# Kernel tuning notes

Measured on AMD Instinct MI355X. Metric: run time of the kernel, lower is better.

The kernel has to match this reference:

```python
import jax, jax.numpy as jnp
import numpy as np

LN_EPS = 1e-5
EPS = 1e-8
MESH_LR = 1.0
MESH_ITERS = 4
SH_ITERS = 5
SA_ITERS = 3


def build_grid(res):
    ranges = [np.linspace(0.0, 1.0, num=r) for r in res]
    g = np.stack(np.meshgrid(*ranges, indexing='ij'), axis=-1)
    g = g.reshape(res[0], res[1], -1)[None]
    return jnp.asarray(np.concatenate([g, 1.0 - g], axis=-1).astype(np.float32))  # [1,H,W,4]


def layer_norm(x, w, b):
    m = jnp.mean(x, axis=-1, keepdims=True)
    v = jnp.var(x, axis=-1, keepdims=True)
    return (x - m) * jax.lax.rsqrt(v + LN_EPS) * w + b


def l2norm(x):
    n = jnp.linalg.norm(x, axis=-1, keepdims=True)
    return x / jnp.maximum(n, 1e-12)  # matches F.normalize eps


def conv_relu(x, w, b, stride):
    y = jax.lax.conv_general_dilated(x, w, (stride, stride), [(2, 2), (2, 2)],
                                     dimension_numbers=('NCHW', 'OIHW', 'NCHW'))
    return jax.nn.relu(y + b[None, :, None, None])


def sinkhorn(C, a, b, u=None, v=None, n_iters=SH_ITERS):
    # log-domain Sinkhorn; C: [B,N,S] cost, a: [B,N], b: [B,S] marginals
    p = -C
    log_a, log_b = jnp.log(a), jnp.log(b)
    if u is None:
        u = jnp.zeros_like(a)
    if v is None:
        v = jnp.zeros_like(b)
    for _ in range(n_iters):
        u = log_a - jax.nn.logsumexp(p + v[:, None, :], axis=2)
        v = log_b - jax.nn.logsumexp(p + u[:, :, None], axis=1)
    pi = jnp.exp(p + u[:, :, None] + v[:, None, :])
    return pi, u, v


def minimize_entropy_of_sinkhorn(C0, a, b, mesh_lr=MESH_LR, n_mesh_iters=MESH_ITERS):
    # gradient descent on the cost matrix to minimize entropy of the transport plan
    def ent(C, u, v):
        pi, u2, v2 = sinkhorn(C, a, b, u=u, v=v)
        e = jnp.mean(-jnp.sum(pi * jnp.log(pi + EPS), axis=(1, 2)))
        return e, (u2, v2)

    grad_fn = jax.grad(ent, has_aux=True)
    u, v = jnp.zeros_like(a), jnp.zeros_like(b)
    C = C0
    for _ in range(n_mesh_iters):
        g, (u, v) = grad_fn(C, u, v)
        C = C - mesh_lr * g
    return C, u, v


def gru_cell(x, h, wih, whh, bih, bhh):
    gi = x @ wih.T + bih
    gh = h @ whh.T + bhh
    ir, iz, inn = jnp.split(gi, 3, axis=-1)
    hr, hz, hn = jnp.split(gh, 3, axis=-1)
    r = jax.nn.sigmoid(ir + hr)
    z = jax.nn.sigmoid(iz + hz)
    n = jnp.tanh(inn + r * hn)
    return (1.0 - z) * n + z * h


def setup_inputs() -> dict:
    key = jax.random.key(0)
    ks = iter(jax.random.split(key, 48))

    def nrm(shape, fan_in):
        return jax.random.normal(next(ks), shape, jnp.float32) / np.sqrt(fan_in).astype(np.float32)

    B, d, S, HID = 16, 64, 8, 128
    z = lambda *s: jnp.zeros(s, jnp.float32)
    o = lambda *s: jnp.ones(s, jnp.float32)
    inp = {
        'image': jax.random.normal(next(ks), (B, 3, 128, 128), jnp.float32),
        'slots_noise': jax.random.normal(next(ks), (B, S, d), jnp.float32),
        'conv1_w': nrm((64, 3, 5, 5), 75), 'conv1_b': z(64),
        'conv2_w': nrm((64, 64, 5, 5), 1600), 'conv2_b': z(64),
        'conv3_w': nrm((64, 64, 5, 5), 1600), 'conv3_b': z(64),
        'conv4_w': nrm((64, 64, 5, 5), 1600), 'conv4_b': z(64),
        'pos_w': nrm((d, 4), 4), 'pos_b': z(d),
        'mlp1_w': nrm((d, d), d), 'mlp1_b': z(d),
        'mlp2_w': nrm((d, d), d), 'mlp2_b': z(d),
        'ln_in_w': o(d), 'ln_in_b': z(d),
        'wk': nrm((d, d), d), 'wv': nrm((d, d), d), 'wq': nrm((d, d), d),
        'mwi_w': nrm((1, d), d), 'mwi_b': z(1),
        'mws_w': nrm((1, d), d), 'mws_b': z(1),
        'ln_sl_w': o(d), 'ln_sl_b': z(d),
        'gru_wih': nrm((3 * d, d), d), 'gru_whh': nrm((3 * d, d), d),
        'gru_bih': z(3 * d), 'gru_bhh': z(3 * d),
        'ln_ff_w': o(d), 'ln_ff_b': z(d),
        'fc1_w': nrm((HID, d), d), 'fc1_b': z(HID),
        'fc2_w': nrm((d, HID), HID), 'fc2_b': z(d),
        'slots_mu': nrm((1, 1, d), d),
        'slots_sigma': jax.random.uniform(next(ks), (1, 1, d), jnp.float32),
        'num_slots': 8,
    }
    return inp


def reference(image, slots_noise, conv1_w, conv1_b, conv2_w, conv2_b, conv3_w, conv3_b,
              conv4_w, conv4_b, pos_w, pos_b, mlp1_w, mlp1_b, mlp2_w, mlp2_b,
              ln_in_w, ln_in_b, wk, wv, wq, mwi_w, mwi_b, mws_w, mws_b,
              ln_sl_w, ln_sl_b, gru_wih, gru_whh, gru_bih, gru_bhh,
              ln_ff_w, ln_ff_b, fc1_w, fc1_b, fc2_w, fc2_b,
              slots_mu, slots_sigma, num_slots):
    B = image.shape[0]
    d = slots_mu.shape[-1]
    # --- CNN encoder (strided_convs=True => latent 32x32) ---
    x = conv_relu(image, conv1_w, conv1_b, 1)
    x = conv_relu(x, conv2_w, conv2_b, 2)
    x = conv_relu(x, conv3_w, conv3_b, 2)
    x = conv_relu(x, conv4_w, conv4_b, 1)          # [B,64,32,32]
    x = x.transpose(0, 2, 3, 1)                    # [B,32,32,64]
    grid = build_grid((32, 32))                    # [1,32,32,4]
    x = x + (grid @ pos_w.T + pos_b)               # soft position embed
    feat = x.reshape(B, -1, d)                     # [B,1024,64]
    # --- pre-slot-attention MLP ---
    feat = jax.nn.relu(feat @ mlp1_w.T + mlp1_b) @ mlp2_w.T + mlp2_b
    # --- slot attention with MESH-Sinkhorn ---
    n_s = num_slots
    slots = slots_mu + (jnp.abs(slots_sigma) + EPS) * slots_noise  # Normal rsample
    inp = layer_norm(feat, ln_in_w, ln_in_b)
    k = inp @ wk.T
    v = inp @ wv.T
    a = jax.nn.softmax((inp @ mwi_w.T + mwi_b).squeeze(-1), axis=-1) * n_s  # [B,N]
    kn = l2norm(k)
    attn = None
    for _ in range(SA_ITERS):
        slots_prev = slots
        s = layer_norm(slots, ln_sl_w, ln_sl_b)
        bm = jax.nn.softmax((s @ mws_w.T + mws_b).squeeze(-1), axis=-1) * n_s  # [B,S]
        q = s @ wq.T
        C = 1.0 - jnp.einsum('bnd,bsd->bns', kn, l2norm(q))  # cosine distance
        C, p, qq = minimize_entropy_of_sinkhorn(C, a, bm)
        pi, _, _ = sinkhorn(C, a, bm, u=p, v=qq)
        attn = pi.transpose(0, 2, 1)                         # [B,S,N]
        updates = jnp.einsum('bsn,bnd->bsd', attn, v)
        slots = gru_cell(updates.reshape(-1, d), slots_prev.reshape(-1, d),
                         gru_wih, gru_whh, gru_bih, gru_bhh).reshape(B, n_s, d)
        h = layer_norm(slots, ln_ff_w, ln_ff_b)
        slots = slots + (jax.nn.relu(h @ fc1_w.T + fc1_b) @ fc2_w.T + fc2_b)
    return slots, attn
```

## Files before the change

### kernel.cpp

```cpp
#include <hip/hip_runtime.h>
#include <hip/hip_bf16.h>


#define LN_EPS 1e-5f
#define SEPS 1e-8f
#define LN8 2.0794415416798357f

__device__ inline float ldf(float x) { return x; }
__device__ inline float ldf(__hip_bfloat16 x) { return __bfloat162float(x); }
__device__ inline void stf(float* p, float v) { *p = v; }
__device__ inline void stf(__hip_bfloat16* p, float v) { *p = __float2bfloat16(v); }

__device__ inline float wmaxall(float v) {
#pragma unroll
  for (int o = 32; o; o >>= 1) v = fmaxf(v, __shfl_down(v, o));
  return __shfl(v, 0);
}
__device__ inline float wsumall(float v) {
#pragma unroll
  for (int o = 32; o; o >>= 1) v += __shfl_down(v, o);
  return __shfl(v, 0);
}
__device__ inline int wsumi(int v) {
#pragma unroll
  for (int o = 32; o; o >>= 1) v += __shfl_down(v, o);
  return __shfl(v, 0);
}
__device__ inline float fast_sigmoid(float x) { return 1.f / (1.f + __expf(-x)); }
__device__ inline float fast_tanh(float x) { return 1.f - 2.f / (__expf(2.f * x) + 1.f); }

__global__ __launch_bounds__(64) void sniff_kernel(const unsigned int* __restrict__ img,
                                                   int* __restrict__ flag) {
  int cnt = 0;
  for (int i = threadIdx.x; i < 512; i += 64) {
    unsigned lo = img[i] & 0xFFFFu;
    int e = (int)((lo >> 7) & 0xFFu);
    cnt += (e >= 96 && e <= 140) ? 1 : 0;
  }
  cnt = wsumi(cnt);
  if (threadIdx.x == 0) *flag = (cnt >= 300) ? 1 : 0;
}

struct CvtArgs {
  const void* src[39];
  long off[40];
};

__global__ __launch_bounds__(256) void convert_kernel(CvtArgs a, const int* __restrict__ flag,
                                                      float* __restrict__ dst, long total) {
  const int isbf = *flag;
  for (long g = (long)blockIdx.x * 256 + threadIdx.x; g < total; g += (long)gridDim.x * 256) {
    int lo = 0, hi = 38;
    while (lo < hi) {
      int mid = (lo + hi + 1) >> 1;
      if (a.off[mid] <= g) lo = mid; else hi = mid - 1;
    }
    long li = g - a.off[lo];
    float v;
    if (isbf) v = __bfloat162float(((const __hip_bfloat16*)a.src[lo])[li]);
    else      v = ((const float*)a.src[lo])[li];
    dst[g] = v;
  }
}

struct TwArgs {
  long soff[9]; long doff[9]; int R[9]; int C[9];
};

__global__ __launch_bounds__(256) void transw_kernel(const float* __restrict__ cvt,
                                                     float* __restrict__ tws, TwArgs a) {
  int m = blockIdx.x;
  const float* S = cvt + a.soff[m];
  float* D = tws + a.doff[m];
  int R = a.R[m], C = a.C[m];
  for (int idx = threadIdx.x; idx < R * C; idx += 256) {
    int i = idx / C, j = idx - i * C;
    D[j * R + i] = S[idx];
  }
}

template <int S, typename TIN, typename TOUT>
__global__ __launch_bounds__(256) void conv5x5(
    const TIN* __restrict__ in, const float* __restrict__ wgt,
    const float* __restrict__ bias, TOUT* __restrict__ out,
    int Cin, int H, int W, int Ho, int Wo, int Cout, int tilesX) {
  constexpr int P = 15 * S + 5;
  constexpr int PP = (S == 1) ? 20 : 40;
  constexpr int NCH = (S == 1) ? 2 : 3;
  constexpr int NP = (P * P + 255) / 256;
  __shared__ __align__(16) float patch[P * PP];
  __shared__ float wt16[25 * 16];
  const int b = blockIdx.z;
  const int ocg = blockIdx.y * 16;
  const int ty0 = (blockIdx.x / tilesX) * 16, tx0 = (blockIdx.x % tilesX) * 16;
  const int og = threadIdx.x >> 6;
  const int r = (threadIdx.x >> 2) & 15;
  const int rx = threadIdx.x & 3;
  const int iy0 = ty0 * S - 2, ix0 = tx0 * S - 2;
  const long HW = (long)H * W;

  int toff[NP], soff[NP];
#pragma unroll
  for (int q = 0; q < NP; q++) {
    int idx = threadIdx.x + 256 * q;
    toff[q] = -1;
    soff[q] = -1;
    if (idx < P * P) {
      int py = idx / P, px = idx - py * P;
      int iy = iy0 + py, ix = ix0 + px;
      int pxs = (S == 2) ? (px ^ (((py >> 1) & 1) << 2)) : px;
      toff[q] = py * PP + pxs;
      if (iy >= 0 && iy < H && ix >= 0 && ix < W) soff[q] = iy * W + ix;
    }
  }
  int wsrc[2];
#pragma unroll
  for (int q = 0; q < 2; q++) {
    int idx = threadIdx.x + 256 * q;
    wsrc[q] = (idx < 400) ? (((ocg + (idx & 15)) * Cin) * 25 + (idx >> 4)) : -1;
  }

  float acc[4][4];
#pragma unroll
  for (int p = 0; p < 4; p++)
#pragma unroll
    for (int j = 0; j < 4; j++) acc[p][j] = 0.f;

  float pr[NP], wr[2];
  {
    const TIN* inp = in + (long)b * Cin * HW;
#pragma unroll
    for (int q = 0; q < NP; q++) pr[q] = (soff[q] >= 0) ? ldf(inp[soff[q]]) : 0.f;
#pragma unroll
    for (int q = 0; q < 2; q++) wr[q] = (wsrc[q] >= 0) ? wgt[wsrc[q]] : 0.f;
  }

  for (int ci = 0; ci < Cin; ++ci) {
    __syncthreads();
#pragma unroll
    for (int q = 0; q < NP; q++)
      if (toff[q] >= 0) patch[toff[q]] = pr[q];
#pragma unroll
    for (int q = 0; q < 2; q++) {
      int idx = threadIdx.x + 256 * q;
      if (idx < 400) wt16[idx] = wr[q];
    }
    __syncthreads();
    if (ci + 1 < Cin) {
      const TIN* inp = in + ((long)b * Cin + ci + 1) * HW;
#pragma unroll
      for (int q = 0; q < NP; q++) pr[q] = (soff[q] >= 0) ? ldf(inp[soff[q]]) : 0.f;
#pragma unroll
      for (int q = 0; q < 2; q++)
        if (wsrc[q] >= 0) wr[q] = wgt[wsrc[q] + (ci + 1) * 25];
    }
#pragma unroll
    for (int ky = 0; ky < 5; ky++) {
      float win[4 * NCH];
      const int row = r * S + ky;
      const float* rb = &patch[row * PP];
      if constexpr (S == 2) {
        const int sw = (row >> 1) & 1;
#pragma unroll
        for (int c = 0; c < NCH; c++) {
          const int g = rx * 2 + c;
          float4 t4 = *(const float4*)(rb + ((g ^ sw) << 2));
          win[4 * c + 0] = t4.x;
          win[4 * c + 1] = t4.y;
          win[4 * c + 2] = t4.z;
          win[4 * c + 3] = t4.w;
        }
      } else {
        const float* bp = rb + rx * 4;
#pragma unroll
        for (int c = 0; c < NCH; c++) {
          float4 t4 = *(const float4*)(bp + 4 * c);
          win[4 * c + 0] = t4.x;
          win[4 * c + 1] = t4.y;
          win[4 * c + 2] = t4.z;
          win[4 * c + 3] = t4.w;
        }
      }
#pragma unroll
      for (int kx = 0; kx < 5; kx++) {
        const float4 wv = *(const float4*)&wt16[(ky * 5 + kx) * 16 + og * 4];
#pragma unroll
        for (int p = 0; p < 4; p++) {
          float iv = win[p * S + kx];
          acc[p][0] += iv * wv.x;
          acc[p][1] += iv * wv.y;
          acc[p][2] += iv * wv.z;
          acc[p][3] += iv * wv.w;
        }
      }
    }
  }
  const int oy = ty0 + r, ox0 = tx0 + rx * 4;
#pragma unroll
  for (int j = 0; j < 4; j++) {
    int oc = ocg + og * 4 + j;
    float bs = bias[oc];
    TOUT* op = &out[(((long)b * Cout + oc) * Ho + oy) * Wo + ox0];
#pragma unroll
    for (int p = 0; p < 4; p++) stf(&op[p], fmaxf(acc[p][j] + bs, 0.f));
  }
}

__global__ __launch_bounds__(64) void token_kernel(
    const float* __restrict__ act4, const float* __restrict__ pos_w,
    const float* __restrict__ pos_b,
    const float* __restrict__ mlp1T, const float* __restrict__ mlp1_b,
    const float* __restrict__ mlp2T, const float* __restrict__ mlp2_b,
    const float* __restrict__ lnin_w, const float* __restrict__ lnin_b,
    const float* __restrict__ wkT, const float* __restrict__ wvT,
    const float* __restrict__ mwi_w, const float* __restrict__ mwi_b,
    float* __restrict__ knT_out, float* __restrict__ v_out, float* __restrict__ lg_out) {
  const int t = blockIdx.x, i = threadIdx.x;
  const int b = t >> 10, nn = t & 1023;
  const int h = nn >> 5, w = nn & 31;
  __shared__ float f[64], h1[64], inp[64];
  {
    float gh = h * (1.f / 31.f), gw = w * (1.f / 31.f);
    float e = gh * pos_w[i * 4 + 0] + gw * pos_w[i * 4 + 1] +
              (1.f - gh) * pos_w[i * 4 + 2] + (1.f - gw) * pos_w[i * 4 + 3] + pos_b[i];
    f[i] = act4[(((long)b * 64 + i) * 32 + h) * 32 + w] + e;
  }
  __syncthreads();
  float acc = 0.f;
  for (int j = 0; j < 64; j++) acc += f[j] * mlp1T[j * 64 + i];
  h1[i] = fmaxf(acc + mlp1_b[i], 0.f);
  __syncthreads();
  acc = 0.f;
  for (int j = 0; j < 64; j++) acc += h1[j] * mlp2T[j * 64 + i];
  float x = acc + mlp2_b[i];
  float m = wsumall(x) * (1.f / 64.f);
  float d0 = x - m;
  float var = wsumall(d0 * d0) * (1.f / 64.f);
  float xin = d0 * rsqrtf(var + LN_EPS) * lnin_w[i] + lnin_b[i];
  inp[i] = xin;
  __syncthreads();
  float kv = 0.f, vv = 0.f;
  for (int j = 0; j < 64; j++) {
    float ij = inp[j];
    kv += ij * wkT[j * 64 + i];
    vv += ij * wvT[j * 64 + i];
  }
  float ss = wsumall(kv * kv);
  knT_out[(long)b * 65536 + i * 1024 + nn] = kv / fmaxf(sqrtf(ss), 1e-12f);
  v_out[(long)t * 64 + i] = vv;
  float lg = wsumall(xin * mwi_w[i]);
  if (i == 0) lg_out[t] = lg + mwi_b[0];
}

__global__ __launch_bounds__(512) void sa_kernel(
    const float* __restrict__ knT_g, const float* __restrict__ v_g,
    const float* __restrict__ la_g, const float* __restrict__ noise,
    const float* __restrict__ mu_w, const float* __restrict__ sg_w,
    const float* __restrict__ lnsl_w, const float* __restrict__ lnsl_b,
    const float* __restrict__ mws_w, const float* __restrict__ mws_b,
    const float* __restrict__ wqT,
    const float* __restrict__ wihT, const float* __restrict__ whhT,
    const float* __restrict__ bih, const float* __restrict__ bhh,
    const float* __restrict__ lnff_w, const float* __restrict__ lnff_b,
    const float* __restrict__ fc1T, const float* __restrict__ fc1_b,
    const float* __restrict__ fc2T, const float* __restrict__ fc2_b,
    float* __restrict__ out) {
  const int b = blockIdx.x, tid = threadIdx.x;
  const int wv = tid >> 6, ln = tid & 63;

  __shared__ float sCt[8192];
  __shared__ float sEc[8192];
  __shared__ float sLa[1024], sELa[1024], sHid[1024];
  __shared__ float sPart[512 * 9];
  __shared__ float sVh[48], sV[8], sEsv[8], sGv[8], sLb[8], sBm[8];
  __shared__ float sC1[8], sEvh[8];
  __shared__ float sSlots[512], sNorm[512], sQn[512], sUpd[512];

  const float* knt = knT_g + (long)b * 65536;
  const float* vf = v_g + (long)b * 65536;
  float sInvH[5][2];
  float gPr[2][8];
  float gInit[2];

  {
    int dd = tid & 63;
    sSlots[tid] = mu_w[dd] + (fabsf(sg_w[dd]) + SEPS) * noise[(long)b * 512 + tid];
  }
  for (int n = tid; n < 1024; n += 512) sLa[n] = la_g[b * 1024 + n];
  __syncthreads();
  {
    float a0 = sLa[tid], a1 = sLa[tid + 512];
    float m0 = wmaxall(fmaxf(a0, a1));
    if (ln == 0) sBm[wv] = m0;
    __syncthreads();
    float M = sBm[0];
#pragma unroll
    for (int s = 1; s < 8; s++) M = fmaxf(M, sBm[s]);
    float e0 = wsumall(__expf(a0 - M) + __expf(a1 - M));
    if (ln == 0) sGv[wv] = e0;
    __syncthreads();
    float SS = 0.f;
#pragma unroll
    for (int s = 0; s < 8; s++) SS += sGv[s];
    float lse = M + __logf(SS);
    float l0 = a0 - lse + LN8, l1 = a1 - lse + LN8;
    sLa[tid] = l0;
    sLa[tid + 512] = l1;
    sELa[tid] = __expf(l0);
    sELa[tid + 512] = __expf(l1);
  }
  __syncthreads();

  for (int it = 0; it < 3; ++it) {
    {
      float x = sSlots[wv * 64 + ln];
      float m = wsumall(x) * (1.f / 64.f);
      float d0 = x - m;
      float var = wsumall(d0 * d0) * (1.f / 64.f);
      float xn = d0 * rsqrtf(var + LN_EPS) * lnsl_w[ln] + lnsl_b[ln];
      sNorm[wv * 64 + ln] = xn;
      float bmv = wsumall(xn * mws_w[ln]);
      if (ln == 0) sBm[wv] = bmv + mws_b[0];
    }
    __syncthreads();
    if (tid == 0) {
      float mx = -1e30f;
      for (int s = 0; s < 8; s++) mx = fmaxf(mx, sBm[s]);
      float ss = 0.f;
      for (int s = 0; s < 8; s++) ss += __expf(sBm[s] - mx);
      float lse = mx + __logf(ss);
      for (int s = 0; s < 8; s++) sLb[s] = sBm[s] - lse + LN8;
    }
    {
      float acc = 0.f;
      for (int j = 0; j < 64; j++) acc += sNorm[wv * 64 + j] * wqT[j * 64 + ln];
      sQn[tid] = acc;
    }
    __syncthreads();
    {
      float qv = sQn[wv * 64 + ln];
      float ss = wsumall(qv * qv);
      sQn[wv * 64 + ln] = qv / fmaxf(sqrtf(ss), 1e-12f);
    }
    if (tid < 8) {
      sV[tid] = 0.f;
      sEsv[tid] = 1.f;
    }
    __syncthreads();

#pragma unroll
    for (int k = 0; k < 2; k++) {
      int n = tid + 512 * k;
      float acc[8];
#pragma unroll
      for (int s = 0; s < 8; s++) acc[s] = 0.f;
      for (int j = 0; j < 64; j++) {
        float kvv = knt[j * 1024 + n];
#pragma unroll
        for (int s = 0; s < 8; s++) acc[s] += kvv * sQn[s * 64 + j];
      }
#pragma unroll
      for (int s = 0; s < 8; s++) {
        float c = 1.f - acc[s];
        sCt[s * 1024 + n] = c;
        sEc[s * 1024 + n] = __expf(-c);
      }
    }
    __syncthreads();

    for (int m = 0; m < 4; m++) {
#pragma unroll
      for (int t = 1; t <= 5; t++) {
        if (t == 1 && tid < 8) sVh[tid] = sV[tid];
        float esv_r[8], part[8];
#pragma unroll
        for (int s = 0; s < 8; s++) { esv_r[s] = sEsv[s]; part[s] = 0.f; }
#pragma unroll
        for (int k = 0; k < 2; k++) {
          int n = tid + 512 * k;
          float ec[8], S = 0.f;
#pragma unroll
          for (int s = 0; s < 8; s++) {
            ec[s] = sEc[s * 1024 + n];
            S += esv_r[s] * ec[s];
          }
          float inv = 1.f / S;
          sInvH[t - 1][k] = inv;
          float w = sELa[n] * inv;
#pragma unroll
          for (int s = 0; s < 8; s++) part[s] += w * ec[s];
        }
#pragma unroll
        for (int s = 0; s < 8; s++) sPart[tid * 9 + s] = part[s];
        __syncthreads();
        {
          int s = wv;
          float acc = 0.f;
#pragma unroll
          for (int q = 0; q < 8; q++) acc += sPart[(ln + 64 * q) * 9 + s];
          acc = wsumall(acc);
          if (ln == 0) {
            float vs = sLb[s] - __logf(acc);
            sV[s] = vs;
            sVh[t * 8 + s] = vs;
            sEsv[s] = __expf(vs);
          }
        }
        __syncthreads();
      }
      {
        float esv_r[8], part[8];
#pragma unroll
        for (int s = 0; s < 8; s++) { esv_r[s] = sEsv[s]; part[s] = 0.f; }
#pragma unroll
        for (int k = 0; k < 2; k++) {
          int n = tid + 512 * k;
          float al = sELa[n] * sInvH[4][k];
          float gul = 0.f;
#pragma unroll
          for (int s = 0; s < 8; s++) {
            float pi = al * esv_r[s] * sEc[s * 1024 + n];
            float gl = -(__logf(pi + SEPS) + pi / (pi + SEPS)) * pi * (1.f / 16.f);
            gPr[k][s] = gl;
            gul += gl;
            part[s] += gl;
          }
          gInit[k] = gul;
        }
#pragma unroll
        for (int s = 0; s < 8; s++) sPart[tid * 9 + s] = part[s];
        __syncthreads();
        {
          int s = wv;
          float acc = 0.f;
#pragma unroll
          for (int q = 0; q < 8; q++) acc += sPart[(ln + 64 * q) * 9 + s];
          acc = wsumall(acc);
          if (ln == 0) {
            sGv[s] = acc;
            sC1[s] = acc * __expf(sVh[40 + s] - sLb[s]);
            sEvh[s] = __expf(sVh[32 + s]);
          }
        }
        __syncthreads();
      }
#pragma unroll
      for (int t = 5; t >= 1; t--) {
        float c1_r[8], evh_r[8], part[8];
#pragma unroll
        for (int s = 0; s < 8; s++) {
          c1_r[s] = sC1[s];
          evh_r[s] = sEvh[s];
          part[s] = 0.f;
        }
#pragma unroll
        for (int k = 0; k < 2; k++) {
          int n = tid + 512 * k;
          float inv = sInvH[t - 1][k];
          float al = sELa[n] * inv;
          float gul = (t == 5) ? gInit[k] : 0.f;
          float ec[8];
#pragma unroll
          for (int s = 0; s < 8; s++) {
            ec[s] = sEc[s * 1024 + n];
            float t2 = al * c1_r[s] * ec[s];
            gPr[k][s] -= t2;
            gul -= t2;
          }
          float bv = gul * inv;
#pragma unroll
          for (int s = 0; s < 8; s++) {
            float pe = bv * ec[s];
            gPr[k][s] -= pe * evh_r[s];
            part[s] += pe;
          }
          if (t == 1) {
#pragma unroll
            for (int s = 0; s < 8; s++) {
              float cn = sCt[s * 1024 + n] + gPr[k][s];
              sCt[s * 1024 + n] = cn;
              sEc[s * 1024 + n] = __expf(-cn);
            }
          }
        }
        if (t > 1) {
#pragma unroll
          for (int s = 0; s < 8; s++) sPart[tid * 9 + s] = part[s];
        }
        if (t == 1 && tid < 8) {
          float vs = sVh[40 + tid];
          sV[tid] = vs;
          sEsv[tid] = __expf(vs);
        }
        __syncthreads();
        if (t > 1) {
          int s = wv;
          float acc = 0.f;
#pragma unroll
          for (int q = 0; q < 8; q++) acc += sPart[(ln + 64 * q) * 9 + s];
          acc = wsumall(acc);
          if (ln == 0) {
            float gn = -evh_r[s] * acc;
            sGv[s] = gn;
            sC1[s] = gn * __expf(sVh[(t - 1) * 8 + s] - sLb[s]);
            sEvh[s] = __expf(sVh[(t - 2) * 8 + s]);
          }
          __syncthreads();
        }
      }
    }

    float invF[2];
    for (int t = 0; t < 5; t++) {
      float esv_r[8], part[8];
#pragma unroll
      for (int s = 0; s < 8; s++) { esv_r[s] = sEsv[s]; part[s] = 0.f; }
#pragma unroll
      for (int k = 0; k < 2; k++) {
        int n = tid + 512 * k;
        float ec[8], S = 0.f;
#pragma unroll
        for (int s = 0; s < 8; s++) {
          ec[s] = sEc[s * 1024 + n];
          S += esv_r[s] * ec[s];
        }
        float inv = 1.f / S;
        invF[k] = inv;
        float w = sELa[n] * inv;
#pragma unroll
        for (int s = 0; s < 8; s++) part[s] += w * ec[s];
      }
#pragma unroll
      for (int s = 0; s < 8; s++) sPart[tid * 9 + s] = part[s];
      __syncthreads();
      {
        int s = wv;
        float acc = 0.f;
#pragma unroll
        for (int q = 0; q < 8; q++) acc += sPart[(ln + 64 * q) * 9 + s];
        acc = wsumall(acc);
        if (ln == 0) {
          float vs = sLb[s] - __logf(acc);
          sV[s] = vs;
          sEsv[s] = __expf(vs);
        }
      }
      __syncthreads();
    }
    {
      float esv_r[8];
#pragma unroll
      for (int s = 0; s < 8; s++) esv_r[s] = sEsv[s];
#pragma unroll
      for (int k = 0; k < 2; k++) {
        int n = tid + 512 * k;
        float al = sELa[n] * invF[k];
#pragma unroll
        for (int s = 0; s < 8; s++)
          sCt[s * 1024 + n] = al * esv_r[s] * sEc[s * 1024 + n];
      }
    }
    __syncthreads();
    if (it == 2) {
      for (int o = tid; o < 8192; o += 512) out[8192 + (long)b * 8192 + o] = sCt[o];
    }
    {
      int s = tid >> 6, dd = tid & 63;
      float acc = 0.f;
      for (int n = 0; n < 1024; n++) acc += sCt[s * 1024 + n] * vf[n * 64 + dd];
      sUpd[tid] = acc;
    }
    __syncthreads();
    float newslot;
    {
      int s = tid >> 6, i = tid & 63;
      const float* x = &sUpd[s * 64];
      const float* h = &sSlots[s * 64];
      float gir = 0, giz = 0, gin = 0, ghr = 0, ghz = 0, ghn = 0;
      for (int j = 0; j < 64; j++) {
        float xv = x[j], hv = h[j];
        gir += xv * wihT[j * 192 + i];
        giz += xv * wihT[j * 192 + 64 + i];
        gin += xv * wihT[j * 192 + 128 + i];
        ghr += hv * whhT[j * 192 + i];
        ghz += hv * whhT[j * 192 + 64 + i];
        ghn += hv * whhT[j * 192 + 128 + i];
      }
      gir += bih[i]; giz += bih[64 + i]; gin += bih[128 + i];
      ghr += bhh[i]; ghz += bhh[64 + i]; ghn += bhh[128 + i];
      float r = fast_sigmoid(gir + ghr);
      float z = fast_sigmoid(giz + ghz);
      float nn = fast_tanh(gin + r * ghn);
      newslot = (1.f - z) * nn + z * h[i];
    }
    __syncthreads();
    sSlots[tid] = newslot;
    __syncthreads();
    {
      float x = sSlots[wv * 64 + ln];
      float m = wsumall(x) * (1.f / 64.f);
      float d0 = x - m;
      float var = wsumall(d0 * d0) * (1.f / 64.f);
      sNorm[wv * 64 + ln] = d0 * rsqrtf(var + LN_EPS) * lnff_w[ln] + lnff_b[ln];
    }
    __syncthreads();
    for (int o = tid; o < 1024; o += 512) {
      int s = o >> 7, k2 = o & 127;
      float acc = 0.f;
      for (int j = 0; j < 64; j++) acc += sNorm[s * 64 + j] * fc1T[j * 128 + k2];
      sHid[o] = fmaxf(acc + fc1_b[k2], 0.f);
    }
    __syncthreads();
    {
      int s = tid >> 6, i = tid & 63;
      float acc = 0.f;
      for (int j = 0; j < 128; j++) acc += sHid[s * 128 + j] * fc2T[j * 64 + i];
      newslot = sSlots[tid] + acc + fc2_b[i];
    }
    __syncthreads();
    sSlots[tid] = newslot;
    __syncthreads();
  }
  out[(long)b * 512 + tid] = sSlots[tid];
}

extern "C" void kernel_launch(void* const* d_in, const int* in_sizes, int n_in,
                              void* d_out, int out_size, void* d_ws, size_t ws_size,
                              hipStream_t stream) {
  (void)n_in; (void)out_size; (void)ws_size;
  char* ws = (char*)d_ws;
  float* cvt  = (float*)ws;
  float* lgts = (float*)(ws + 5570560ull);
  __hip_bfloat16* act1 = (__hip_bfloat16*)(ws + 5636096ull);
  __hip_bfloat16* act2 = (__hip_bfloat16*)(ws + 39190528ull);
  float* act3 = (float*)(ws + 5636096ull);
  float* act4 = (float*)(ws + 9830400ull);
  float* knT  = (float*)(ws + 14024704ull);
  float* vf   = (float*)(ws + 18219008ull);
  int*   flag = (int*)(ws + 47579136ull);
  float* tws  = (float*)(ws + 47583232ull);

  CvtArgs ca;
  long total = 0;
  for (int i = 0; i < 39; i++) { ca.src[i] = d_in[i]; ca.off[i] = total; total += in_sizes[i]; }
  ca.off[39] = total;

  sniff_kernel<<<1, 64, 0, stream>>>((const unsigned int*)d_in[0], flag);
  convert_kernel<<<1024, 256, 0, stream>>>(ca, flag, cvt, total);

#define ARR(i) (cvt + ca.off[i])
  TwArgs ta;
  {
    const int src[9] = {12, 14, 18, 19, 20, 27, 28, 33, 35};
    const int R[9] = {64, 64, 64, 64, 64, 192, 192, 128, 64};
    const int C[9] = {64, 64, 64, 64, 64, 64, 64, 64, 128};
    long d = 0;
    for (int m2 = 0; m2 < 9; m2++) {
      ta.soff[m2] = ca.off[src[m2]];
      ta.doff[m2] = d;
      ta.R[m2] = R[m2];
      ta.C[m2] = C[m2];
      d += (long)R[m2] * C[m2];
    }
  }
  transw_kernel<<<9, 256, 0, stream>>>(cvt, tws, ta);
  float* mlp1T = tws + 0,     *mlp2T = tws + 4096,  *wkT = tws + 8192, *wvT = tws + 12288;
  float* wqT   = tws + 16384, *wihT  = tws + 20480, *whhT = tws + 32768;
  float* fc1T  = tws + 45056, *fc2T  = tws + 53248;

  const float* image = ARR(0);
  const float* noise = ARR(1);

  conv5x5<1, float, __hip_bfloat16><<<dim3(64, 4, 16), 256, 0, stream>>>(
      image, ARR(2), ARR(3), act1, 3, 128, 128, 128, 128, 64, 8);
  conv5x5<2, __hip_bfloat16, __hip_bfloat16><<<dim3(16, 4, 16), 256, 0, stream>>>(
      act1, ARR(4), ARR(5), act2, 64, 128, 128, 64, 64, 64, 4);
  conv5x5<2, __hip_bfloat16, float><<<dim3(4, 4, 16), 256, 0, stream>>>(
      act2, ARR(6), ARR(7), act3, 64, 64, 64, 32, 32, 64, 2);
  conv5x5<1, float, float><<<dim3(4, 4, 16), 256, 0, stream>>>(
      act3, ARR(8), ARR(9), act4, 64, 32, 32, 32, 32, 64, 2);

  token_kernel<<<16384, 64, 0, stream>>>(act4, ARR(10), ARR(11),
                                         mlp1T, ARR(13), mlp2T, ARR(15),
                                         ARR(16), ARR(17), wkT, wvT, ARR(21), ARR(22),
                                         knT, vf, lgts);

  sa_kernel<<<16, 512, 0, stream>>>(knT, vf, lgts, noise, ARR(37), ARR(38),
                                    ARR(25), ARR(26), ARR(23), ARR(24), wqT,
                                    wihT, whhT, ARR(29), ARR(30),
                                    ARR(31), ARR(32), fc1T, ARR(34), fc2T, ARR(36),
                                    (float*)d_out);
#undef ARR
}
```

Measured before the change: 956.2 us.

## Replace two-barrier shared reductions with wave shuffles and double-buffered partials

Each Sinkhorn step and gradient step previously wrote per-thread partials to a large shared array, synchronized, reduced per slot in one wave, wrote scalars back and synchronized again. Now each wave reduces its eight partials with shuffles and writes eight values into a double-buffered 64-entry shared array. After a single barrier every thread redundantly sums the eight wave results and keeps the dual variables in registers, in exp form instead of log form. The change also uses hardware reciprocal instead of division and precomputes exp(lb) and exp(-lb), trading some accuracy and extra shuffle work for half the barriers and less shared-memory traffic.

```diff
diff --git a/kernel.cpp b/kernel.cpp
--- a/kernel.cpp
+++ b/kernel.cpp
@@ -10,6 +10,7 @@
 __device__ inline float ldf(__hip_bfloat16 x) { return __bfloat162float(x); }
 __device__ inline void stf(float* p, float v) { *p = v; }
 __device__ inline void stf(__hip_bfloat16* p, float v) { *p = __float2bfloat16(v); }
+__device__ inline float frcp(float x) { return __builtin_amdgcn_rcpf(x); }
 
 __device__ inline float wmaxall(float v) {
 #pragma unroll
@@ -270,10 +271,11 @@
 
   __shared__ float sCt[8192];
   __shared__ float sEc[8192];
-  __shared__ float sLa[1024], sELa[1024], sHid[1024];
-  __shared__ float sPart[512 * 9];
-  __shared__ float sVh[48], sV[8], sEsv[8], sGv[8], sLb[8], sBm[8];
-  __shared__ float sC1[8], sEvh[8];
+  __shared__ float sLa[1024];
+  __shared__ float sELa[1024], sHid[1024];
+  __shared__ __align__(16) float sWp[2][64];
+  __shared__ __align__(16) float sEh[48];
+  __shared__ float sLb[8], sELb[8], sRLb[8], sBm[8], sTmp[8];
   __shared__ float sSlots[512], sNorm[512], sQn[512], sUpd[512];
 
   const float* knt = knT_g + (long)b * 65536;
@@ -281,6 +283,9 @@
   float sInvH[5][2];
   float gPr[2][8];
   float gInit[2];
+  float esv_r[8];
+  float c1_r[8], evh_r[8];
+  int pp = 0;
 
   {
     int dd = tid & 63;
@@ -297,17 +302,14 @@
 #pragma unroll
     for (int s = 1; s < 8; s++) M = fmaxf(M, sBm[s]);
     float e0 = wsumall(__expf(a0 - M) + __expf(a1 - M));
-    if (ln == 0) sGv[wv] = e0;
+    if (ln == 0) sTmp[wv] = e0;
     __syncthreads();
     float SS = 0.f;
 #pragma unroll
-    for (int s = 0; s < 8; s++) SS += sGv[s];
+    for (int s = 0; s < 8; s++) SS += sTmp[s];
     float lse = M + __logf(SS);
-    float l0 = a0 - lse + LN8, l1 = a1 - lse + LN8;
-    sLa[tid] = l0;
-    sLa[tid + 512] = l1;
-    sELa[tid] = __expf(l0);
-    sELa[tid + 512] = __expf(l1);
+    sELa[tid] = __expf(a0 - lse + LN8);
+    sELa[tid + 512] = __expf(a1 - lse + LN8);
   }
   __syncthreads();
 
@@ -329,7 +331,12 @@
       float ss = 0.f;
       for (int s = 0; s < 8; s++) ss += __expf(sBm[s] - mx);
       float lse = mx + __logf(ss);
-      for (int s = 0; s < 8; s++) sLb[s] = sBm[s] - lse + LN8;
+      for (int s = 0; s < 8; s++) {
+        float lb = sBm[s] - lse + LN8;
+        sLb[s] = lb;
+        sELb[s] = __expf(lb);
+        sRLb[s] = __expf(-lb);
+      }
     }
     {
       float acc = 0.f;
@@ -341,10 +348,6 @@
       float qv = sQn[wv * 64 + ln];
       float ss = wsumall(qv * qv);
       sQn[wv * 64 + ln] = qv / fmaxf(sqrtf(ss), 1e-12f);
-    }
-    if (tid < 8) {
-      sV[tid] = 0.f;
-      sEsv[tid] = 1.f;
     }
     __syncthreads();
 
@@ -366,15 +369,20 @@
         sEc[s * 1024 + n] = __expf(-c);
       }
     }
+#pragma unroll
+    for (int s = 0; s < 8; s++) esv_r[s] = 1.f;
     __syncthreads();
 
     for (int m = 0; m < 4; m++) {
 #pragma unroll
       for (int t = 1; t <= 5; t++) {
-        if (t == 1 && tid < 8) sVh[tid] = sV[tid];
-        float esv_r[8], part[8];
-#pragma unroll
-        for (int s = 0; s < 8; s++) { esv_r[s] = sEsv[s]; part[s] = 0.f; }
+        if (t == 1 && tid == 0) {
+#pragma unroll
+          for (int s = 0; s < 8; s++) sEh[s] = esv_r[s];
+        }
+        float part[8];
+#pragma unroll
+        for (int s = 0; s < 8; s++) part[s] = 0.f;
 #pragma unroll
         for (int k = 0; k < 2; k++) {
           int n = tid + 512 * k;
@@ -384,34 +392,35 @@
             ec[s] = sEc[s * 1024 + n];
             S += esv_r[s] * ec[s];
           }
-          float inv = 1.f / S;
+          float inv = frcp(S);
           sInvH[t - 1][k] = inv;
           float w = sELa[n] * inv;
 #pragma unroll
           for (int s = 0; s < 8; s++) part[s] += w * ec[s];
         }
 #pragma unroll
-        for (int s = 0; s < 8; s++) sPart[tid * 9 + s] = part[s];
+        for (int s = 0; s < 8; s++) part[s] = wsumall(part[s]);
+        if (ln == 0) {
+#pragma unroll
+          for (int s = 0; s < 8; s++) sWp[pp][s * 8 + wv] = part[s];
+        }
         __syncthreads();
-        {
-          int s = wv;
-          float acc = 0.f;
-#pragma unroll
-          for (int q = 0; q < 8; q++) acc += sPart[(ln + 64 * q) * 9 + s];
-          acc = wsumall(acc);
-          if (ln == 0) {
-            float vs = sLb[s] - __logf(acc);
-            sV[s] = vs;
-            sVh[t * 8 + s] = vs;
-            sEsv[s] = __expf(vs);
-          }
-        }
-        __syncthreads();
+#pragma unroll
+        for (int s = 0; s < 8; s++) {
+          const float* q = &sWp[pp][s * 8];
+          float a = ((q[0] + q[1]) + (q[2] + q[3])) + ((q[4] + q[5]) + (q[6] + q[7]));
+          esv_r[s] = sELb[s] * frcp(a);
+        }
+        if (tid == 0) {
+#pragma unroll
+          for (int s = 0; s < 8; s++) sEh[t * 8 + s] = esv_r[s];
+        }
+        pp ^= 1;
       }
       {
-        float esv_r[8], part[8];
-#pragma unroll
-        for (int s = 0; s < 8; s++) { esv_r[s] = sEsv[s]; part[s] = 0.f; }
+        float part[8];
+#pragma unroll
+        for (int s = 0; s < 8; s++) part[s] = 0.f;
 #pragma unroll
         for (int k = 0; k < 2; k++) {
           int n = tid + 512 * k;
@@ -420,7 +429,8 @@
 #pragma unroll
           for (int s = 0; s < 8; s++) {
             float pi = al * esv_r[s] * sEc[s * 1024 + n];
-            float gl = -(__logf(pi + SEPS) + pi / (pi + SEPS)) * pi * (1.f / 16.f);
+            float ps = pi + SEPS;
+            float gl = -(__logf(ps) + pi * frcp(ps)) * pi * (1.f / 16.f);
             gPr[k][s] = gl;
             gul += gl;
             part[s] += gl;
@@ -428,31 +438,26 @@
           gInit[k] = gul;
         }
 #pragma unroll
-        for (int s = 0; s < 8; s++) sPart[tid * 9 + s] = part[s];
+        for (int s = 0; s < 8; s++) part[s] = wsumall(part[s]);
+        if (ln == 0) {
+#pragma unroll
+          for (int s = 0; s < 8; s++) sWp[pp][s * 8 + wv] = part[s];
+        }
         __syncthreads();
-        {
-          int s = wv;
-          float acc = 0.f;
-#pragma unroll
-          for (int q = 0; q < 8; q++) acc += sPart[(ln + 64 * q) * 9 + s];
-          acc = wsumall(acc);
-          if (ln == 0) {
-            sGv[s] = acc;
-            sC1[s] = acc * __expf(sVh[40 + s] - sLb[s]);
-            sEvh[s] = __expf(sVh[32 + s]);
-          }
-        }
-        __syncthreads();
+#pragma unroll
+        for (int s = 0; s < 8; s++) {
+          const float* q = &sWp[pp][s * 8];
+          float gv = ((q[0] + q[1]) + (q[2] + q[3])) + ((q[4] + q[5]) + (q[6] + q[7]));
+          c1_r[s] = gv * sEh[40 + s] * sRLb[s];
+          evh_r[s] = sEh[32 + s];
+        }
+        pp ^= 1;
       }
 #pragma unroll
       for (int t = 5; t >= 1; t--) {
-        float c1_r[8], evh_r[8], part[8];
-#pragma unroll
-        for (int s = 0; s < 8; s++) {
-          c1_r[s] = sC1[s];
-          evh_r[s] = sEvh[s];
-          part[s] = 0.f;
-        }
+        float part[8];
+#pragma unroll
+        for (int s = 0; s < 8; s++) part[s] = 0.f;
 #pragma unroll
         for (int k = 0; k < 2; k++) {
           int n = tid + 512 * k;
@@ -485,36 +490,35 @@
         }
         if (t > 1) {
 #pragma unroll
-          for (int s = 0; s < 8; s++) sPart[tid * 9 + s] = part[s];
-        }
-        if (t == 1 && tid < 8) {
-          float vs = sVh[40 + tid];
-          sV[tid] = vs;
-          sEsv[tid] = __expf(vs);
+          for (int s = 0; s < 8; s++) part[s] = wsumall(part[s]);
+          if (ln == 0) {
+#pragma unroll
+            for (int s = 0; s < 8; s++) sWp[pp][s * 8 + wv] = part[s];
+          }
         }
         __syncthreads();
         if (t > 1) {
-          int s = wv;
-          float acc = 0.f;
-#pragma unroll
-          for (int q = 0; q < 8; q++) acc += sPart[(ln + 64 * q) * 9 + s];
-          acc = wsumall(acc);
-          if (ln == 0) {
-            float gn = -evh_r[s] * acc;
-            sGv[s] = gn;
-            sC1[s] = gn * __expf(sVh[(t - 1) * 8 + s] - sLb[s]);
-            sEvh[s] = __expf(sVh[(t - 2) * 8 + s]);
+#pragma unroll
+          for (int s = 0; s < 8; s++) {
+            const float* q = &sWp[pp][s * 8];
+            float a = ((q[0] + q[1]) + (q[2] + q[3])) + ((q[4] + q[5]) + (q[6] + q[7]));
+            float gn = -evh_r[s] * a;
+            c1_r[s] = gn * sEh[(t - 1) * 8 + s] * sRLb[s];
+            evh_r[s] = sEh[(t - 2) * 8 + s];
           }
-          __syncthreads();
+          pp ^= 1;
+        } else {
+#pragma unroll
+          for (int s = 0; s < 8; s++) esv_r[s] = sEh[40 + s];
         }
       }
     }
 
     float invF[2];
-    for (int t = 0; t < 5; t++) {
-      float esv_r[8], part[8];
-#pragma unroll
-      for (int s = 0; s < 8; s++) { esv_r[s] = sEsv[s]; part[s] = 0.f; }
+    for (int tt = 0; tt < 5; tt++) {
+      float part[8];
+#pragma unroll
+      for (int s = 0; s < 8; s++) part[s] = 0.f;
 #pragma unroll
       for (int k = 0; k < 2; k++) {
         int n = tid + 512 * k;
@@ -524,33 +528,28 @@
           ec[s] = sEc[s * 1024 + n];
           S += esv_r[s] * ec[s];
         }
-        float inv = 1.f / S;
+        float inv = frcp(S);
         invF[k] = inv;
         float w = sELa[n] * inv;
 #pragma unroll
         for (int s = 0; s < 8; s++) part[s] += w * ec[s];
       }
 #pragma unroll
-      for (int s = 0; s < 8; s++) sPart[tid * 9 + s] = part[s];
+      for (int s = 0; s < 8; s++) part[s] = wsumall(part[s]);
+      if (ln == 0) {
+#pragma unroll
+        for (int s = 0; s < 8; s++) sWp[pp][s * 8 + wv] = part[s];
+      }
       __syncthreads();
-      {
-        int s = wv;
-        float acc = 0.f;
-#pragma unroll
-        for (int q = 0; q < 8; q++) acc += sPart[(ln + 64 * q) * 9 + s];
-        acc = wsumall(acc);
-        if (ln == 0) {
-          float vs = sLb[s] - __logf(acc);
-          sV[s] = vs;
-          sEsv[s] = __expf(vs);
-        }
-      }
-      __syncthreads();
-    }
-    {
-      float esv_r[8];
-#pragma unroll
-      for (int s = 0; s < 8; s++) esv_r[s] = sEsv[s];
+#pragma unroll
+      for (int s = 0; s < 8; s++) {
+        const float* q = &sWp[pp][s * 8];
+        float a = ((q[0] + q[1]) + (q[2] + q[3])) + ((q[4] + q[5]) + (q[6] + q[7]));
+        esv_r[s] = sELb[s] * frcp(a);
+      }
+      pp ^= 1;
+    }
+    {
 #pragma unroll
       for (int k = 0; k < 2; k++) {
         int n = tid + 512 * k;
```

Measured after the change: 1.077 ms. 12.7% more time.
